# Optimization experiments

Hardware: AMD Instinct MI355X
Metric: run time of the kernel (lower is better)

Reference implementation:

```python
import jax, jax.numpy as jnp
import numpy as np

DIM = 112        # input channels
DIM_OUT = 224    # output channels (stage transition)
HEADS = 4
HD = DIM_OUT // HEADS          # 56
WS = 8                         # window size before query pooling
QS = 2                         # query_stride
MLP_DIM = int(DIM_OUT * 4.0)   # 896
EPS = 1e-6
SCALE = HD ** -0.5


def _layernorm(x, g, b):
    m = x.mean(-1, keepdims=True)
    d = x - m
    v = (d * d).mean(-1, keepdims=True)
    return d * jax.lax.rsqrt(v + EPS) * g + b


def _maxpool2(x):
    # stride==pool_size max pooling via reshape (NHWC)
    B, H, W, C = x.shape
    return x.reshape(B, H // QS, QS, W // QS, QS, C).max(axis=(2, 4))


def setup_inputs() -> dict:
    key = jax.random.key(0)
    ks = jax.random.split(key, 8)
    def n(k, s, sc=0.02):
        return jax.random.normal(k, s, dtype=jnp.float32) * sc
    return {
        "hidden_states": jax.random.normal(ks[0], (8, 128, 128, DIM), dtype=jnp.float32),
        "ln1_g": jnp.ones((DIM,), jnp.float32),
        "ln1_b": jnp.zeros((DIM,), jnp.float32),
        "qkv_w": n(ks[1], (DIM, 3 * DIM_OUT)),
        "qkv_b": jnp.zeros((3 * DIM_OUT,), jnp.float32),
        "attn_proj_w": n(ks[2], (DIM_OUT, DIM_OUT)),
        "attn_proj_b": jnp.zeros((DIM_OUT,), jnp.float32),
        "res_proj_w": n(ks[3], (DIM, DIM_OUT)),
        "res_proj_b": jnp.zeros((DIM_OUT,), jnp.float32),
        "ln2_g": jnp.ones((DIM_OUT,), jnp.float32),
        "ln2_b": jnp.zeros((DIM_OUT,), jnp.float32),
        "mlp1_w": n(ks[4], (DIM_OUT, MLP_DIM)),
        "mlp1_b": jnp.zeros((MLP_DIM,), jnp.float32),
        "mlp2_w": n(ks[5], (MLP_DIM, DIM_OUT)),
        "mlp2_b": jnp.zeros((DIM_OUT,), jnp.float32),
    }


def reference(hidden_states, ln1_g, ln1_b, qkv_w, qkv_b, attn_proj_w, attn_proj_b,
              res_proj_w, res_proj_b, ln2_g, ln2_b, mlp1_w, mlp1_b, mlp2_w, mlp2_b):
    x = hidden_states
    B, H, W, _ = x.shape  # H, W divisible by WS -> no padding branch needed
    hs = _layernorm(x, ln1_g, ln1_b)
    # dim != dim_out: residual = pooled projection of normed input
    residual = _maxpool2(hs @ res_proj_w + res_proj_b)  # (B, H/2, W/2, DIM_OUT)

    # window partition: (B*nh*nw, WS, WS, DIM)
    nh, nw = H // WS, W // WS
    w = hs.reshape(B, nh, WS, nw, WS, DIM).transpose(0, 1, 3, 2, 4, 5)
    w = w.reshape(B * nh * nw, WS, WS, DIM)

    # multi-scale attention with query pooling
    qkv = (w @ qkv_w + qkv_b).reshape(-1, WS * WS, 3, HEADS, HD)
    q, k, v = qkv[:, :, 0], qkv[:, :, 1], qkv[:, :, 2]
    q = _maxpool2(q.reshape(-1, WS, WS, DIM_OUT))          # (Bw, WS/2, WS/2, DIM_OUT)
    q = q.reshape(-1, (WS // QS) ** 2, HEADS, HD)
    q = q.transpose(0, 2, 1, 3)   # (Bw, h, Lq, d)
    k = k.transpose(0, 2, 1, 3)   # (Bw, h, Lk, d)
    v = v.transpose(0, 2, 1, 3)
    attn = jax.nn.softmax(jnp.einsum('bhqd,bhkd->bhqk', q * SCALE, k), axis=-1)
    o = jnp.einsum('bhqk,bhkd->bhqd', attn, v).transpose(0, 2, 1, 3)
    ws2 = WS // QS
    o = o.reshape(-1, ws2, ws2, DIM_OUT)
    o = o @ attn_proj_w + attn_proj_b

    # window unpartition at pooled resolution
    H2, W2 = H // QS, W // QS
    o = o.reshape(B, nh, nw, ws2, ws2, DIM_OUT).transpose(0, 1, 3, 2, 4, 5)
    o = o.reshape(B, H2, W2, DIM_OUT)

    hs = residual + o
    ln = _layernorm(hs, ln2_g, ln2_b)
    mlp = jax.nn.gelu(ln @ mlp1_w + mlp1_b, approximate=False) @ mlp2_w + mlp2_b
    return hs + mlp
```

## Files before the change

kernel.cpp:

```cpp
#include <hip/hip_runtime.h>
#include <hip/hip_bf16.h>
#include <math.h>


#define SCALE_A 0.13363062095621219f

typedef __attribute__((ext_vector_type(8))) short short8;
typedef __attribute__((ext_vector_type(4))) short short4v;
typedef __attribute__((ext_vector_type(4))) float f32x4;
typedef __attribute__((ext_vector_type(16))) float f32x16;

__device__ inline short f2bf(float x) {
  union { float f; unsigned u; } v; v.f = x;
  unsigned r = v.u + 0x7fff + ((v.u >> 16) & 1);
  return (short)(r >> 16);
}
__device__ inline float gelu_fast(float x) {
  float x2 = x * x;
  float p = fmaf(x2, 0.044715f, 1.0f);
  float t = -1.5957691216057308f * x * p;
  return x / (1.0f + __expf(t));
}

__global__ void cast_w_kernel(const float* __restrict__ qkv_w,
                              const float* __restrict__ rp_w,
                              const float* __restrict__ ap_w,
                              const float* __restrict__ m1_w,
                              const float* __restrict__ m2_w,
                              short* __restrict__ wF) {
  int tid = blockIdx.x * blockDim.x + threadIdx.x;
  int stride = gridDim.x * blockDim.x;
  for (int e = tid; e < 90112; e += stride) {
    int j = e & 7, lr = (e >> 3) & 15, lqq = (e >> 7) & 3, tile = e >> 9;
    int kt = tile & 3, nt = tile >> 2;
    int cp = nt * 16 + lr;
    int h = cp / 176, cl = cp % 176;
    int k = kt * 32 + lqq * 8 + j;
    float val = 0.f;
    if (k < 112 && cl < 168) {
      int bcol = (cl < 56) ? (h * 56 + cl)
               : (cl < 112) ? (224 + h * 56 + (cl - 56))
                            : (448 + h * 56 + (cl - 112));
      val = qkv_w[k * 672 + bcol];
    }
    wF[e] = f2bf(val);
  }
  for (int e = tid; e < 28672; e += stride) {
    int j = e & 7, lr = (e >> 3) & 15, lqq = (e >> 7) & 3, tile = e >> 9;
    int kt = tile & 3, nt = tile >> 2;
    int n = nt * 16 + lr, k = kt * 32 + lqq * 8 + j;
    wF[90112 + e] = (k < 112) ? f2bf(rp_w[k * 224 + n]) : (short)0;
  }
  for (int e = tid; e < 50176; e += stride) {
    int j = e & 7, lr = (e >> 3) & 15, lqq = (e >> 7) & 3, tile = e >> 9;
    int kt = tile % 7, nt = tile / 7;
    int n = nt * 16 + lr, k = kt * 32 + lqq * 8 + j;
    wF[118784 + e] = f2bf(ap_w[k * 224 + n]);
  }
  for (int e = tid; e < 200704; e += stride) {
    int j = e & 7, lane = (e >> 3) & 63, unit = e >> 9;
    int kt = unit % 14, nt = unit / 14;
    int n = nt * 32 + (lane & 31), k = kt * 16 + (lane >> 5) * 8 + j;
    wF[168960 + e] = f2bf(m1_w[k * 896 + n]);
  }
  for (int e = tid; e < 200704; e += stride) {
    int j = e & 7, lane = (e >> 3) & 63, unit = e >> 9;
    int kt = unit % 56, nt = unit / 56;
    int n = nt * 32 + (lane & 31), k = kt * 16 + (lane >> 5) * 8 + j;
    wF[369664 + e] = f2bf(m2_w[k * 224 + n]);
  }
}

__global__ __launch_bounds__(256) void ln1_kernel(
    const float* __restrict__ x, const float* __restrict__ g,
    const float* __restrict__ b, short* __restrict__ hs) {
  int wave = threadIdx.x >> 6, lane = threadIdx.x & 63;
  int half = lane >> 5, sub = lane & 31;
  size_t row = (size_t)blockIdx.x * 8 + wave * 2 + half;
  const float* rp = x + row * 112;
  f32x4 v = {0.f, 0.f, 0.f, 0.f};
  if (sub < 28) v = *(const f32x4*)(rp + sub * 4);
  float s = v[0] + v[1] + v[2] + v[3];
  #pragma unroll
  for (int off = 16; off; off >>= 1) s += __shfl_xor(s, off, 32);
  float mean = s * (1.f / 112.f);
  float s2 = 0.f;
  #pragma unroll
  for (int q = 0; q < 4; ++q) { float d = v[q] - mean; s2 = fmaf(d, d, s2); }
  if (sub >= 28) s2 = 0.f;
  #pragma unroll
  for (int off = 16; off; off >>= 1) s2 += __shfl_xor(s2, off, 32);
  float rs = rsqrtf(s2 * (1.f / 112.f) + 1e-6f);
  if (sub < 28) {
    f32x4 gg = *(const f32x4*)(g + sub * 4);
    f32x4 bb = *(const f32x4*)(b + sub * 4);
    short4v o;
    #pragma unroll
    for (int q = 0; q < 4; ++q)
      o[q] = f2bf((v[q] - mean) * rs * gg[q] + bb[q]);
    *(short4v*)(hs + row * 112 + sub * 4) = o;
  }
}

__global__ __launch_bounds__(256, 8) void respool_kernel(
    const short* __restrict__ hs, const short* __restrict__ rpF,
    const float* __restrict__ bias, float* __restrict__ hs2) {
  __shared__ alignas(16) short w_s[64 * 136];
  int blk = blockIdx.x;
  int tid = threadIdx.x;
  for (int e = tid; e < 1024; e += 256) {
    int m = e >> 4, c = e & 15;
    short8* dst = (short8*)&w_s[m * 136 + c * 8];
    if (c < 14) {
      int p = m >> 2, r = m & 3;
      int pix = blk * 16 + p;
      int bb = pix >> 12, ii = (pix >> 6) & 63, jj = pix & 63;
      size_t token = ((size_t)(bb * 128 + 2 * ii + (r >> 1))) * 128 + 2 * jj + (r & 1);
      *dst = *(const short8*)(hs + token * 112 + c * 8);
    } else {
      short8 z = {0, 0, 0, 0, 0, 0, 0, 0};
      *dst = z;
    }
  }
  __syncthreads();
  int wave = tid >> 6, lane = tid & 63, lrow = lane & 15, lq = lane >> 4;
  short8 Ar[4];
  #pragma unroll
  for (int kt = 0; kt < 4; ++kt)
    Ar[kt] = *(const short8*)&w_s[(wave * 16 + lrow) * 136 + kt * 32 + lq * 8];
  int p = wave * 4 + lq;
  for (int pr = 0; pr < 7; ++pr) {
    int c0 = pr * 32 + lrow, c1 = c0 + 16;
    f32x4 acc0 = {0.f, 0.f, 0.f, 0.f}, acc1 = {0.f, 0.f, 0.f, 0.f};
    #pragma unroll
    for (int kt = 0; kt < 4; ++kt) {
      short8 b0 = *(const short8*)(rpF + (((2 * pr) * 4 + kt) * 64 + lane) * 8);
      short8 b1 = *(const short8*)(rpF + (((2 * pr + 1) * 4 + kt) * 64 + lane) * 8);
      acc0 = __builtin_amdgcn_mfma_f32_16x16x32_bf16(Ar[kt], b0, acc0, 0, 0, 0);
      acc1 = __builtin_amdgcn_mfma_f32_16x16x32_bf16(Ar[kt], b1, acc1, 0, 0, 0);
    }
    float m0 = fmaxf(fmaxf(acc0[0], acc0[1]), fmaxf(acc0[2], acc0[3])) + bias[c0];
    float m1 = fmaxf(fmaxf(acc1[0], acc1[1]), fmaxf(acc1[2], acc1[3])) + bias[c1];
    hs2[(size_t)(blk * 16 + p) * 224 + c0] = m0;
    hs2[(size_t)(blk * 16 + p) * 224 + c1] = m1;
  }
}

__global__ __launch_bounds__(256, 2) void attn_kernel(
    const short* __restrict__ hs, const short* __restrict__ qkvF,
    const float* __restrict__ qkv_b, const short* __restrict__ apF,
    const float* __restrict__ apb, float* __restrict__ hs2) {
  __shared__ alignas(16) short u_s[4 * 9792];
  int win = blockIdx.x;
  int nw = win & 15, nh = (win >> 4) & 15, b = win >> 8;
  int tid = threadIdx.x;
  int wave = tid >> 6, lane = tid & 63, lrow = lane & 15, lq = lane >> 4;
  short* w_s  = u_s;
  short* k_s  = u_s + wave * 9792;
  short* vT_s = k_s + 4608;
  short* qp_s = k_s + 8640;

  for (int e = tid; e < 1024; e += 256) {
    int m = e >> 4, c = e & 15;
    short8* dst = (short8*)&w_s[m * 136 + c * 8];
    if (c < 14) {
      int p = m >> 2, r = m & 3;
      int tr = (p >> 2) * 2 + (r >> 1), tc = (p & 3) * 2 + (r & 1);
      size_t token = ((size_t)(b * 128 + nh * 8 + tr)) * 128 + (nw * 8 + tc);
      *dst = *(const short8*)(hs + token * 112 + c * 8);
    } else {
      short8 z = {0, 0, 0, 0, 0, 0, 0, 0};
      *dst = z;
    }
  }
  __syncthreads();

  short8 Aw[4][4];
  #pragma unroll
  for (int mt = 0; mt < 4; ++mt)
    #pragma unroll
    for (int kt = 0; kt < 4; ++kt)
      Aw[mt][kt] = *(const short8*)&w_s[(mt * 16 + lrow) * 136 + kt * 32 + lq * 8];
  __syncthreads();

  {
    short8 z = {0, 0, 0, 0, 0, 0, 0, 0};
    *(short8*)&k_s[lane * 72 + 56] = z;
    if (lane < 16) *(short8*)&qp_s[lane * 72 + 56] = z;
  }

  int h = wave;

  #pragma unroll 2
  for (int t = 0; t < 11; ++t) {
    int cl = t * 16 + lrow;
    f32x4 ac[4] = {{0.f,0.f,0.f,0.f},{0.f,0.f,0.f,0.f},
                   {0.f,0.f,0.f,0.f},{0.f,0.f,0.f,0.f}};
    short8 bw[4];
    #pragma unroll
    for (int kt = 0; kt < 4; ++kt)
      bw[kt] = *(const short8*)(qkvF + (((h * 11 + t) * 4 + kt) * 64 + lane) * 8);
    #pragma unroll
    for (int kt = 0; kt < 4; ++kt)
      #pragma unroll
      for (int mt = 0; mt < 4; ++mt)
        ac[mt] = __builtin_amdgcn_mfma_f32_16x16x32_bf16(Aw[mt][kt], bw[kt], ac[mt], 0, 0, 0);
    if (cl < 56) {
      float bias = qkv_b[h * 56 + cl];
      #pragma unroll
      for (int mt = 0; mt < 4; ++mt) {
        float mx = fmaxf(fmaxf(ac[mt][0], ac[mt][1]),
                         fmaxf(ac[mt][2], ac[mt][3])) + bias;
        qp_s[(mt * 4 + lq) * 72 + cl] = f2bf(mx * SCALE_A);
      }
    } else if (cl < 112) {
      float bias = qkv_b[224 + h * 56 + (cl - 56)];
      #pragma unroll
      for (int mt = 0; mt < 4; ++mt)
        #pragma unroll
        for (int r = 0; r < 4; ++r)
          k_s[(mt * 16 + lq * 4 + r) * 72 + (cl - 56)] = f2bf(ac[mt][r] + bias);
    } else if (cl < 168) {
      float bias = qkv_b[448 + h * 56 + (cl - 112)];
      #pragma unroll
      for (int mt = 0; mt < 4; ++mt) {
        short4v pk = {f2bf(ac[mt][0] + bias), f2bf(ac[mt][1] + bias),
                      f2bf(ac[mt][2] + bias), f2bf(ac[mt][3] + bias)};
        *(short4v*)&vT_s[(cl - 112) * 72 + mt * 16 + lq * 4] = pk;
      }
    }
  }

  short8 aq[2];
  #pragma unroll
  for (int kt = 0; kt < 2; ++kt)
    aq[kt] = *(const short8*)&qp_s[lrow * 72 + kt * 32 + lq * 8];
  f32x4 sc[4];
  #pragma unroll
  for (int t = 0; t < 4; ++t) {
    sc[t][0] = sc[t][1] = sc[t][2] = sc[t][3] = 0.f;
    #pragma unroll
    for (int kt = 0; kt < 2; ++kt) {
      short8 bk = *(const short8*)&k_s[(t * 16 + lrow) * 72 + kt * 32 + lq * 8];
      sc[t] = __builtin_amdgcn_mfma_f32_16x16x32_bf16(aq[kt], bk, sc[t], 0, 0, 0);
    }
  }
  float mr[4], sr[4];
  #pragma unroll
  for (int r = 0; r < 4; ++r)
    mr[r] = fmaxf(fmaxf(sc[0][r], sc[1][r]), fmaxf(sc[2][r], sc[3][r]));
  #pragma unroll
  for (int off = 8; off; off >>= 1)
    #pragma unroll
    for (int r = 0; r < 4; ++r) mr[r] = fmaxf(mr[r], __shfl_xor(mr[r], off, 16));
  #pragma unroll
  for (int r = 0; r < 4; ++r) {
    #pragma unroll
    for (int t = 0; t < 4; ++t) sc[t][r] = __expf(sc[t][r] - mr[r]);
    sr[r] = sc[0][r] + sc[1][r] + sc[2][r] + sc[3][r];
  }
  #pragma unroll
  for (int off = 8; off; off >>= 1)
    #pragma unroll
    for (int r = 0; r < 4; ++r) sr[r] += __shfl_xor(sr[r], off, 16);
  #pragma unroll
  for (int r = 0; r < 4; ++r) sr[r] = 1.f / sr[r];
  #pragma unroll
  for (int t = 0; t < 4; ++t)
    #pragma unroll
    for (int r = 0; r < 4; ++r)
      qp_s[(lq * 4 + r) * 72 + t * 16 + lrow] = f2bf(sc[t][r] * sr[r]);

  short8 ap[2];
  #pragma unroll
  for (int kt = 0; kt < 2; ++kt)
    ap[kt] = *(const short8*)&qp_s[lrow * 72 + kt * 32 + lq * 8];
  #pragma unroll
  for (int ct = 0; ct < 4; ++ct) {
    int c0 = (ct < 3) ? ct * 16 : 40;
    int col = c0 + lrow;
    f32x4 ov = {0.f, 0.f, 0.f, 0.f};
    #pragma unroll
    for (int kt = 0; kt < 2; ++kt) {
      short8 bv = *(const short8*)&vT_s[col * 72 + kt * 32 + lq * 8];
      ov = __builtin_amdgcn_mfma_f32_16x16x32_bf16(ap[kt], bv, ov, 0, 0, 0);
    }
    if (ct < 3 || lrow >= 8) {
      #pragma unroll
      for (int r = 0; r < 4; ++r)
        qp_s[(lq * 4 + r) * 72 + col] = f2bf(ov[r]);
    }
  }
  __syncthreads();

  short8 Ao[7];
  #pragma unroll
  for (int kt = 0; kt < 7; ++kt) {
    int c = kt * 32 + lq * 8;
    int h2 = (c >= 168) ? 3 : (c >= 112) ? 2 : (c >= 56) ? 1 : 0;
    Ao[kt] = *(const short8*)&u_s[h2 * 9792 + 8640 + lrow * 72 + (c - h2 * 56)];
  }
  int nt0 = (wave < 2) ? wave * 4 : 8 + (wave - 2) * 3;
  int ncnt2 = (wave < 2) ? 4 : 3;
  for (int i = 0; i < ncnt2; ++i) {
    int nt = nt0 + i;
    f32x4 acc = {0.f, 0.f, 0.f, 0.f};
    #pragma unroll
    for (int kt = 0; kt < 7; ++kt) {
      short8 bw = *(const short8*)(apF + ((nt * 7 + kt) * 64 + lane) * 8);
      acc = __builtin_amdgcn_mfma_f32_16x16x32_bf16(Ao[kt], bw, acc, 0, 0, 0);
    }
    int col2 = nt * 16 + lrow;
    float bi = apb[col2];
    #pragma unroll
    for (int r = 0; r < 4; ++r) {
      size_t token = ((size_t)(b * 64 + nh * 4 + lq)) * 64 + nw * 4 + r;
      float* p = &hs2[token * 224 + col2];
      *p += acc[r] + bi;
    }
  }
}

template <int NT>
__device__ __forceinline__ void mlp1_tiles(
    int nt0, const short* ln_s, const short* __restrict__ m1F,
    const float* __restrict__ b1, short* hid_s, int nl, int half, int lane) {
  f32x16 acc[NT];
  #pragma unroll
  for (int i = 0; i < NT; ++i)
    #pragma unroll
    for (int r = 0; r < 16; ++r) acc[i][r] = 0.f;
  #pragma unroll
  for (int kt = 0; kt < 14; ++kt) {
    short8 a = *(const short8*)&ln_s[nl * 232 + kt * 16 + half * 8];
    #pragma unroll
    for (int i = 0; i < NT; ++i) {
      short8 bw = *(const short8*)(m1F + ((size_t)((nt0 + i) * 14 + kt) * 64 + lane) * 8);
      acc[i] = __builtin_amdgcn_mfma_f32_32x32x16_bf16(a, bw, acc[i], 0, 0, 0);
    }
  }
  #pragma unroll
  for (int i = 0; i < NT; ++i) {
    int col = (nt0 + i) * 32 + nl;
    float bi = b1[col];
    #pragma unroll
    for (int r = 0; r < 16; ++r) {
      int row = (r & 3) + 8 * (r >> 2) + 4 * half;
      hid_s[row * 904 + col] = f2bf(gelu_fast(acc[i][r] + bi));
    }
  }
}

__global__ __launch_bounds__(512, 4) void mlp_kernel(
    const float* __restrict__ hs2, const float* __restrict__ g2,
    const float* __restrict__ b2, const short* __restrict__ m1F,
    const float* __restrict__ b1, const short* __restrict__ m2F,
    const float* __restrict__ b2b, float* __restrict__ out) {
  __shared__ alignas(16) short ln_s[32 * 232];
  __shared__ alignas(16) short hid_s[32 * 904];
  int blk = blockIdx.x;
  int tid = threadIdx.x;
  size_t base = (size_t)blk * 32 * 224;
  {
    int row = tid >> 4, l = tid & 15;
    const float* rp = hs2 + base + (size_t)row * 224;
    float v[14];
    float s = 0.f;
    #pragma unroll
    for (int c = 0; c < 14; ++c) { v[c] = rp[l + 16 * c]; s += v[c]; }
    #pragma unroll
    for (int off = 8; off; off >>= 1) s += __shfl_xor(s, off, 16);
    float mean = s * (1.f / 224.f);
    float s2 = 0.f;
    #pragma unroll
    for (int c = 0; c < 14; ++c) { float d = v[c] - mean; s2 = fmaf(d, d, s2); }
    #pragma unroll
    for (int off = 8; off; off >>= 1) s2 += __shfl_xor(s2, off, 16);
    float rs = rsqrtf(s2 * (1.f / 224.f) + 1e-6f);
    #pragma unroll
    for (int c = 0; c < 14; ++c) {
      int cc = l + 16 * c;
      ln_s[row * 232 + cc] = f2bf((v[c] - mean) * rs * g2[cc] + b2[cc]);
    }
  }
  __syncthreads();
  int wave = tid >> 6, lane = tid & 63;
  int nl = lane & 31, half = lane >> 5;
  if (wave < 4) mlp1_tiles<4>(wave * 4, ln_s, m1F, b1, hid_s, nl, half, lane);
  else          mlp1_tiles<3>(16 + (wave - 4) * 3, ln_s, m1F, b1, hid_s, nl, half, lane);
  __syncthreads();
  if (wave < 7) {
    int nt = wave;
    int col = nt * 32 + nl;
    float res[16];
    #pragma unroll
    for (int r = 0; r < 16; ++r) {
      int row = (r & 3) + 8 * (r >> 2) + 4 * half;
      res[r] = hs2[base + (size_t)row * 224 + col];
    }
    f32x16 ac0 = {0.f,0.f,0.f,0.f,0.f,0.f,0.f,0.f,0.f,0.f,0.f,0.f,0.f,0.f,0.f,0.f};
    f32x16 ac1 = {0.f,0.f,0.f,0.f,0.f,0.f,0.f,0.f,0.f,0.f,0.f,0.f,0.f,0.f,0.f,0.f};
    #pragma unroll 4
    for (int kt = 0; kt < 56; kt += 2) {
      short8 a0 = *(const short8*)&hid_s[nl * 904 + kt * 16 + half * 8];
      short8 a1 = *(const short8*)&hid_s[nl * 904 + (kt + 1) * 16 + half * 8];
      short8 b0 = *(const short8*)(m2F + ((size_t)(nt * 56 + kt) * 64 + lane) * 8);
      short8 b1 = *(const short8*)(m2F + ((size_t)(nt * 56 + kt + 1) * 64 + lane) * 8);
      ac0 = __builtin_amdgcn_mfma_f32_32x32x16_bf16(a0, b0, ac0, 0, 0, 0);
      ac1 = __builtin_amdgcn_mfma_f32_32x32x16_bf16(a1, b1, ac1, 0, 0, 0);
    }
    float bi = b2b[col];
    #pragma unroll
    for (int r = 0; r < 16; ++r) {
      int row = (r & 3) + 8 * (r >> 2) + 4 * half;
      size_t idx = base + (size_t)row * 224 + col;
      out[idx] = res[r] + ac0[r] + ac1[r] + bi;
    }
  }
}

extern "C" void kernel_launch(void* const* d_in, const int* in_sizes, int n_in,
                              void* d_out, int out_size, void* d_ws, size_t ws_size,
                              hipStream_t stream) {
  const float* x    = (const float*)d_in[0];
  const float* ln1g = (const float*)d_in[1];
  const float* ln1b = (const float*)d_in[2];
  const float* qkvw = (const float*)d_in[3];
  const float* qkvb = (const float*)d_in[4];
  const float* apw  = (const float*)d_in[5];
  const float* apb  = (const float*)d_in[6];
  const float* rpw  = (const float*)d_in[7];
  const float* rpb  = (const float*)d_in[8];
  const float* ln2g = (const float*)d_in[9];
  const float* ln2b = (const float*)d_in[10];
  const float* w1   = (const float*)d_in[11];
  const float* b1   = (const float*)d_in[12];
  const float* w2   = (const float*)d_in[13];
  const float* b2   = (const float*)d_in[14];
  float* out = (float*)d_out;

  short* hs_bf = (short*)d_ws;
  float* hs2   = (float*)((char*)d_ws + 29360128);
  short* wF    = (short*)((char*)d_ws + 73400320);

  cast_w_kernel<<<1024, 256, 0, stream>>>(qkvw, rpw, apw, w1, w2, wF);
  ln1_kernel<<<16384, 256, 0, stream>>>(x, ln1g, ln1b, hs_bf);
  respool_kernel<<<2048, 256, 0, stream>>>(hs_bf, wF + 90112, rpb, hs2);
  attn_kernel<<<2048, 256, 0, stream>>>(hs_bf, wF, qkvb, wF + 118784, apb, hs2);
  mlp_kernel<<<1024, 512, 0, stream>>>(hs2, ln2g, ln2b, wF + 168960, b1,
                                       wF + 369664, b2, out);
}
```

Before: 252.1 us.

## Fuse residual projection and max-pool into attention kernel

Removes the separate respool kernel and computes the residual projection plus 2x2 max-pool inside the attention kernel, reusing the window's A fragments already loaded for QKV. The pooled residual is staged in shared memory and added in the output projection epilogue. This replaces the read-modify-write of hs2 with a plain store, saving one kernel launch, one re-read of hs_bf and one hs2 round trip. In exchange the attention kernel does more MFMA work and needs more registers per block.

```diff
diff --git a/kernel.cpp b/kernel.cpp
--- a/kernel.cpp
+++ b/kernel.cpp
@@ -102,54 +102,11 @@
   }
 }
 
-__global__ __launch_bounds__(256, 8) void respool_kernel(
-    const short* __restrict__ hs, const short* __restrict__ rpF,
-    const float* __restrict__ bias, float* __restrict__ hs2) {
-  __shared__ alignas(16) short w_s[64 * 136];
-  int blk = blockIdx.x;
-  int tid = threadIdx.x;
-  for (int e = tid; e < 1024; e += 256) {
-    int m = e >> 4, c = e & 15;
-    short8* dst = (short8*)&w_s[m * 136 + c * 8];
-    if (c < 14) {
-      int p = m >> 2, r = m & 3;
-      int pix = blk * 16 + p;
-      int bb = pix >> 12, ii = (pix >> 6) & 63, jj = pix & 63;
-      size_t token = ((size_t)(bb * 128 + 2 * ii + (r >> 1))) * 128 + 2 * jj + (r & 1);
-      *dst = *(const short8*)(hs + token * 112 + c * 8);
-    } else {
-      short8 z = {0, 0, 0, 0, 0, 0, 0, 0};
-      *dst = z;
-    }
-  }
-  __syncthreads();
-  int wave = tid >> 6, lane = tid & 63, lrow = lane & 15, lq = lane >> 4;
-  short8 Ar[4];
-  #pragma unroll
-  for (int kt = 0; kt < 4; ++kt)
-    Ar[kt] = *(const short8*)&w_s[(wave * 16 + lrow) * 136 + kt * 32 + lq * 8];
-  int p = wave * 4 + lq;
-  for (int pr = 0; pr < 7; ++pr) {
-    int c0 = pr * 32 + lrow, c1 = c0 + 16;
-    f32x4 acc0 = {0.f, 0.f, 0.f, 0.f}, acc1 = {0.f, 0.f, 0.f, 0.f};
-    #pragma unroll
-    for (int kt = 0; kt < 4; ++kt) {
-      short8 b0 = *(const short8*)(rpF + (((2 * pr) * 4 + kt) * 64 + lane) * 8);
-      short8 b1 = *(const short8*)(rpF + (((2 * pr + 1) * 4 + kt) * 64 + lane) * 8);
-      acc0 = __builtin_amdgcn_mfma_f32_16x16x32_bf16(Ar[kt], b0, acc0, 0, 0, 0);
-      acc1 = __builtin_amdgcn_mfma_f32_16x16x32_bf16(Ar[kt], b1, acc1, 0, 0, 0);
-    }
-    float m0 = fmaxf(fmaxf(acc0[0], acc0[1]), fmaxf(acc0[2], acc0[3])) + bias[c0];
-    float m1 = fmaxf(fmaxf(acc1[0], acc1[1]), fmaxf(acc1[2], acc1[3])) + bias[c1];
-    hs2[(size_t)(blk * 16 + p) * 224 + c0] = m0;
-    hs2[(size_t)(blk * 16 + p) * 224 + c1] = m1;
-  }
-}
-
 __global__ __launch_bounds__(256, 2) void attn_kernel(
     const short* __restrict__ hs, const short* __restrict__ qkvF,
     const float* __restrict__ qkv_b, const short* __restrict__ apF,
-    const float* __restrict__ apb, float* __restrict__ hs2) {
+    const float* __restrict__ apb, const short* __restrict__ rpF,
+    const float* __restrict__ rpb, float* __restrict__ hs2) {
   __shared__ alignas(16) short u_s[4 * 9792];
   int win = blockIdx.x;
   int nw = win & 15, nh = (win >> 4) & 15, b = win >> 8;
@@ -293,6 +250,31 @@
   }
   __syncthreads();
 
+  float* res_s = (float*)u_s;
+  int nt0 = (wave < 2) ? wave * 4 : 8 + (wave - 2) * 3;
+  int ncnt2 = (wave < 2) ? 4 : 3;
+  for (int i = 0; i < ncnt2; ++i) {
+    int nt = nt0 + i;
+    f32x4 racc[4] = {{0.f,0.f,0.f,0.f},{0.f,0.f,0.f,0.f},
+                     {0.f,0.f,0.f,0.f},{0.f,0.f,0.f,0.f}};
+    short8 rw[4];
+    #pragma unroll
+    for (int kt = 0; kt < 4; ++kt)
+      rw[kt] = *(const short8*)(rpF + (((nt * 4) + kt) * 64 + lane) * 8);
+    #pragma unroll
+    for (int kt = 0; kt < 4; ++kt)
+      #pragma unroll
+      for (int mt = 0; mt < 4; ++mt)
+        racc[mt] = __builtin_amdgcn_mfma_f32_16x16x32_bf16(Aw[mt][kt], rw[kt], racc[mt], 0, 0, 0);
+    float bi = rpb[nt * 16 + lrow];
+    #pragma unroll
+    for (int mt = 0; mt < 4; ++mt) {
+      float mx = fmaxf(fmaxf(racc[mt][0], racc[mt][1]),
+                       fmaxf(racc[mt][2], racc[mt][3])) + bi;
+      res_s[(mt * 4 + lq) * 228 + nt * 16 + lrow] = mx;
+    }
+  }
+
   short8 Ao[7];
   #pragma unroll
   for (int kt = 0; kt < 7; ++kt) {
@@ -300,8 +282,6 @@
     int h2 = (c >= 168) ? 3 : (c >= 112) ? 2 : (c >= 56) ? 1 : 0;
     Ao[kt] = *(const short8*)&u_s[h2 * 9792 + 8640 + lrow * 72 + (c - h2 * 56)];
   }
-  int nt0 = (wave < 2) ? wave * 4 : 8 + (wave - 2) * 3;
-  int ncnt2 = (wave < 2) ? 4 : 3;
   for (int i = 0; i < ncnt2; ++i) {
     int nt = nt0 + i;
     f32x4 acc = {0.f, 0.f, 0.f, 0.f};
@@ -314,9 +294,9 @@
     float bi = apb[col2];
     #pragma unroll
     for (int r = 0; r < 4; ++r) {
+      float res = res_s[(lq * 4 + r) * 228 + col2];
       size_t token = ((size_t)(b * 64 + nh * 4 + lq)) * 64 + nw * 4 + r;
-      float* p = &hs2[token * 224 + col2];
-      *p += acc[r] + bi;
+      hs2[token * 224 + col2] = res + acc[r] + bi;
     }
   }
 }
@@ -445,8 +425,8 @@
 
   cast_w_kernel<<<1024, 256, 0, stream>>>(qkvw, rpw, apw, w1, w2, wF);
   ln1_kernel<<<16384, 256, 0, stream>>>(x, ln1g, ln1b, hs_bf);
-  respool_kernel<<<2048, 256, 0, stream>>>(hs_bf, wF + 90112, rpb, hs2);
-  attn_kernel<<<2048, 256, 0, stream>>>(hs_bf, wF, qkvb, wF + 118784, apb, hs2);
+  attn_kernel<<<2048, 256, 0, stream>>>(hs_bf, wF, qkvb, wF + 118784, apb,
+                                        wF + 90112, rpb, hs2);
   mlp_kernel<<<1024, 512, 0, stream>>>(hs2, ln2g, ln2b, wF + 168960, b1,
                                        wF + 369664, b2, out);
 }
```

After: 232.8 us. 1.08x faster.
